# Performance work log

Hardware: AMD Instinct MI355X
Metric: run time of the kernel (lower is better)

## Reference

```python
import jax, jax.numpy as jnp
import numpy as np

B, S, D = 2, 2048, 1024
H = 16
HD = D // H


def setup_inputs() -> dict:
    key = jax.random.key(0)
    k = jax.random.split(key, 5)
    s = 0.02
    return {
        "x": jax.random.normal(k[0], (B, S, D), jnp.float32),
        "w_qkv": jax.random.normal(k[1], (3 * D, D), jnp.float32) * s,
        "b_qkv": jax.random.normal(k[2], (3 * D,), jnp.float32) * s,
        "w_out": jax.random.normal(k[3], (D, D), jnp.float32) * s,
        "b_out": jax.random.normal(k[4], (D,), jnp.float32) * s,
    }


def reference(x, w_qkv, b_qkv, w_out, b_out):
    b, s, d = x.shape
    h, hd = H, HD
    scale = hd ** -0.5
    # QKV projection: [B,S,3D] -> [3,B,H,S,hd]
    qkv = x @ w_qkv.T + b_qkv
    qkv = qkv.reshape(b, s, 3, h, hd).transpose(2, 0, 3, 1, 4)
    q, k, v = qkv[0], qkv[1], qkv[2]
    # Attention scores [B,H,S,S]
    scores = jnp.einsum("bhqd,bhkd->bhqk", q, k) * scale
    attn = jax.nn.softmax(scores, axis=-1)
    # Attend and merge heads
    attended = jnp.einsum("bhqk,bhkd->bqhd", attn, v).reshape(b, s, d)
    return attended @ w_out.T + b_out
```

## Files before the change

kernel.cpp:

```cpp
#include <hip/hip_runtime.h>
#include <hip/hip_bf16.h>

typedef __hip_bfloat16 bf16;
typedef __attribute__((ext_vector_type(8))) short short8;
typedef __attribute__((ext_vector_type(8))) __bf16 bf16x8;
typedef __attribute__((ext_vector_type(4))) float f32x4;
typedef __attribute__((ext_vector_type(16))) float f32x16;
typedef __attribute__((ext_vector_type(4))) unsigned int u32x4;
typedef __attribute__((ext_vector_type(2))) unsigned int u32x2;

#define MFMA16(a, b, c)                                                        \
  __builtin_amdgcn_mfma_f32_16x16x32_bf16(__builtin_bit_cast(bf16x8, (a)),     \
                                          __builtin_bit_cast(bf16x8, (b)),     \
                                          (c), 0, 0, 0)
#define MFMA32(a, b, c)                                                        \
  __builtin_amdgcn_mfma_f32_32x32x16_bf16(__builtin_bit_cast(bf16x8, (a)),     \
                                          __builtin_bit_cast(bf16x8, (b)),     \
                                          (c), 0, 0, 0)

#define GLD16(gsrc, ldst)                                                      \
  __builtin_amdgcn_global_load_lds(                                            \
      (const __attribute__((address_space(1))) void*)(gsrc),                   \
      (__attribute__((address_space(3))) void*)(ldst), 16, 0, 0)

__device__ inline short f2bfs(float f) {
  return __builtin_bit_cast(short, __float2bfloat16(f));
}
__device__ inline unsigned pk2(float lo, float hi) {
  unsigned a = (unsigned short)__builtin_bit_cast(short, __float2bfloat16(lo));
  unsigned b = (unsigned short)__builtin_bit_cast(short, __float2bfloat16(hi));
  return a | (b << 16);
}

template <typename T> __device__ inline short8 ld8bf(const T* p);
template <> __device__ inline short8 ld8bf<bf16>(const bf16* p) {
  return *(const short8*)p;
}
template <> __device__ inline short8 ld8bf<float>(const float* p) {
  f32x4 a = *(const f32x4*)p;
  f32x4 b = *(const f32x4*)(p + 4);
  short8 r;
  r[0] = f2bfs(a[0]); r[1] = f2bfs(a[1]); r[2] = f2bfs(a[2]); r[3] = f2bfs(a[3]);
  r[4] = f2bfs(b[0]); r[5] = f2bfs(b[1]); r[6] = f2bfs(b[2]); r[7] = f2bfs(b[3]);
  return r;
}

template <typename OT> __device__ inline void st1(OT* p, float v);
template <> __device__ inline void st1<bf16>(bf16* p, float v) {
  *p = __float2bfloat16(v);
}
template <> __device__ inline void st1<float>(float* p, float v) { *p = v; }

__device__ inline unsigned int funnel16(unsigned int hi, unsigned int lo) {
  return (unsigned int)(((((unsigned long long)hi) << 32) | lo) >> 16);
}
__device__ inline short8 rotl8(short8 v, int r) {
  u32x4 W = __builtin_bit_cast(u32x4, v);
  u32x4 T, U, F;
  int wr = r >> 1;
  T[0] = (wr & 1) ? W[1] : W[0];
  T[1] = (wr & 1) ? W[2] : W[1];
  T[2] = (wr & 1) ? W[3] : W[2];
  T[3] = (wr & 1) ? W[0] : W[3];
  U[0] = (wr & 2) ? T[2] : T[0];
  U[1] = (wr & 2) ? T[3] : T[1];
  U[2] = (wr & 2) ? T[0] : T[2];
  U[3] = (wr & 2) ? T[1] : T[3];
  F[0] = (r & 1) ? funnel16(U[1], U[0]) : U[0];
  F[1] = (r & 1) ? funnel16(U[2], U[1]) : U[1];
  F[2] = (r & 1) ? funnel16(U[3], U[2]) : U[2];
  F[3] = (r & 1) ? funnel16(U[0], U[3]) : U[3];
  return __builtin_bit_cast(short8, F);
}

__global__ __launch_bounds__(256) void cvt3(
    const float* __restrict__ s0, bf16* __restrict__ d0, int n0,
    const float* __restrict__ s1, bf16* __restrict__ d1, int n1,
    const float* __restrict__ s2, bf16* __restrict__ d2, int n2) {
  int i = (blockIdx.x * 256 + threadIdx.x) * 8;
  if (i < n0) {
    *(short8*)&d0[i] = ld8bf(s0 + i);
  } else if ((i -= n0) < n1) {
    *(short8*)&d1[i] = ld8bf(s1 + i);
  } else if ((i -= n1) < n2) {
    *(short8*)&d2[i] = ld8bf(s2 + i);
  }
}

template <typename OT>
__global__ __launch_bounds__(256, 2) void gemm_lds_bias(
    const bf16* __restrict__ A, const bf16* __restrict__ B,
    const float* __restrict__ bias, OT* __restrict__ C, int M, int N, int K) {
  __shared__ bf16 As[128][64];
  __shared__ bf16 Bs[128][64];

  const int tid = threadIdx.x;
  const int w = tid >> 6, l = tid & 63;
  const int wr = w >> 1, wc = w & 1;
  const int m0 = blockIdx.y * 128, n0 = blockIdx.x * 128;

  f32x4 acc[4][4] = {};

  const int srow = l >> 3;
  const int scol = (l & 7) * 8;

  for (int kt = 0; kt < K; kt += 64) {
#pragma unroll
    for (int j = 0; j < 4; ++j) {
      int chunk = w * 4 + j;
      int row = chunk * 8 + srow;
      GLD16(A + (size_t)(m0 + row) * K + kt + scol, &As[0][0] + chunk * 512);
      GLD16(B + (size_t)(n0 + row) * K + kt + scol, &Bs[0][0] + chunk * 512);
    }
    __syncthreads();

#pragma unroll
    for (int kk = 0; kk < 2; ++kk) {
      short8 af[4], bfv[4];
#pragma unroll
      for (int i = 0; i < 4; ++i) {
        af[i]  = *(const short8*)&As[wr * 64 + i * 16 + (l & 15)]
                                   [kk * 32 + (l >> 4) * 8];
        bfv[i] = *(const short8*)&Bs[wc * 64 + i * 16 + (l & 15)]
                                   [kk * 32 + (l >> 4) * 8];
      }
#pragma unroll
      for (int i = 0; i < 4; ++i)
#pragma unroll
        for (int jn = 0; jn < 4; ++jn)
          acc[i][jn] = MFMA16(af[i], bfv[jn], acc[i][jn]);
    }
    __syncthreads();
  }

#pragma unroll
  for (int i = 0; i < 4; ++i) {
    int rbase = m0 + wr * 64 + i * 16 + (l >> 4) * 4;
#pragma unroll
    for (int jn = 0; jn < 4; ++jn) {
      int col = n0 + wc * 64 + jn * 16 + (l & 15);
      float bv = bias[col];
#pragma unroll
      for (int r = 0; r < 4; ++r)
        st1(&C[(size_t)(rbase + r) * N + col], acc[i][jn][r] + bv);
    }
  }
}

template <typename AT, typename OT>
__global__ __launch_bounds__(256, 2) void gemm_bt_bias(
    const AT* __restrict__ A, const float* __restrict__ B,
    const float* __restrict__ bias, OT* __restrict__ C, int M, int N, int K) {
  __shared__ bf16 As[128][64];
  __shared__ bf16 Bs[128][64];

  const int tid = threadIdx.x;
  const int w = tid >> 6, l = tid & 63;
  const int wr = w >> 1, wc = w & 1;
  const int m0 = blockIdx.y * 128, n0 = blockIdx.x * 128;

  f32x4 acc[4][4] = {};

  const int srow = tid >> 3;
  const int scol = (tid & 7) * 8;

  for (int kt = 0; kt < K; kt += 64) {
    short8 aReg[4], bReg[4];
#pragma unroll
    for (int p = 0; p < 4; ++p) {
      int row = p * 32 + srow;
      aReg[p] = ld8bf(A + (size_t)(m0 + row) * K + kt + scol);
      bReg[p] = ld8bf(B + (size_t)(n0 + row) * K + kt + scol);
    }
    __syncthreads();
#pragma unroll
    for (int p = 0; p < 4; ++p) {
      int row = p * 32 + srow;
      *(short8*)&As[row][scol] = aReg[p];
      *(short8*)&Bs[row][scol] = bReg[p];
    }
    __syncthreads();

#pragma unroll
    for (int kk = 0; kk < 2; ++kk) {
      short8 af[4], bfv[4];
#pragma unroll
      for (int i = 0; i < 4; ++i) {
        af[i]  = *(const short8*)&As[wr * 64 + i * 16 + (l & 15)]
                                   [kk * 32 + (l >> 4) * 8];
        bfv[i] = *(const short8*)&Bs[wc * 64 + i * 16 + (l & 15)]
                                   [kk * 32 + (l >> 4) * 8];
      }
#pragma unroll
      for (int i = 0; i < 4; ++i)
#pragma unroll
        for (int jn = 0; jn < 4; ++jn)
          acc[i][jn] = MFMA16(af[i], bfv[jn], acc[i][jn]);
    }
  }

#pragma unroll
  for (int i = 0; i < 4; ++i) {
    int rbase = m0 + wr * 64 + i * 16 + (l >> 4) * 4;
#pragma unroll
    for (int jn = 0; jn < 4; ++jn) {
      int col = n0 + wc * 64 + jn * 16 + (l & 15);
      float bv = bias[col];
#pragma unroll
      for (int r = 0; r < 4; ++r)
        st1(&C[(size_t)(rbase + r) * N + col], acc[i][jn][r] + bv);
    }
  }
}

__global__ __launch_bounds__(256, 2) void attn_fwd(
    const bf16* __restrict__ qkv, bf16* __restrict__ attended) {
  const int S = 2048, D3 = 3072, D = 1024;
  const int qt = blockIdx.x, bh = blockIdx.y;
  const int b = bh >> 4, h = bh & 15;
  const int tid = threadIdx.x, w = tid >> 6, l = tid & 63;
  const int lo5 = l & 31, hi = l >> 5;

  __shared__ bf16 Klds[64][72];
  __shared__ bf16 Vt[64][72];

  const int q0w = qt * 128 + w * 32;

  short8 qf[4];
  {
    size_t qrow = (size_t)(b * S + q0w + lo5) * D3 + h * 64;
#pragma unroll
    for (int ks = 0; ks < 4; ++ks)
      qf[ks] = *(const short8*)&qkv[qrow + ks * 16 + hi * 8];
  }

  float m_raw = -1e30f, l_i = 0.f;
  f32x16 o0 = {}, o1 = {};

  const float Cs = 0.125f * 1.44269504088896340736f;

  const int srow = tid >> 2;
  const int scq = tid & 3;

  short8 k0, k1, v0, v1;
  {
    size_t gb = (size_t)(b * S + srow) * D3 + h * 64 + scq * 16;
    k0 = *(const short8*)&qkv[gb + 1024];
    k1 = *(const short8*)&qkv[gb + 1024 + 8];
    v0 = *(const short8*)&qkv[gb + 2048];
    v1 = *(const short8*)&qkv[gb + 2048 + 8];
  }

  for (int kv0 = 0; kv0 < S; kv0 += 64) {
    __syncthreads();
    *(short8*)&Klds[srow][scq * 16] = k0;
    *(short8*)&Klds[srow][scq * 16 + 8] = k1;
#pragma unroll
    for (int g = 0; g < 2; ++g) {
      int sI = scq * 2 + g;
      short8 u = rotl8(g ? v1 : v0, sI);
#pragma unroll
      for (int j = 0; j < 8; ++j) {
        int jj = (j + sI) & 7;
        *(short*)&Vt[sI * 8 + jj][srow] = (short)u[j];
      }
    }
    __syncthreads();

    if (kv0 + 64 < S) {
      size_t gb = (size_t)(b * S + kv0 + 64 + srow) * D3 + h * 64 + scq * 16;
      k0 = *(const short8*)&qkv[gb + 1024];
      k1 = *(const short8*)&qkv[gb + 1024 + 8];
      v0 = *(const short8*)&qkv[gb + 2048];
      v1 = *(const short8*)&qkv[gb + 2048 + 8];
    }

    f32x16 s0 = {}, s1 = {};
    __builtin_amdgcn_s_setprio(1);
#pragma unroll
    for (int ks = 0; ks < 4; ++ks) {
      short8 ka0 = *(const short8*)&Klds[lo5][ks * 16 + hi * 8];
      short8 ka1 = *(const short8*)&Klds[32 + lo5][ks * 16 + hi * 8];
      s0 = MFMA32(ka0, qf[ks], s0);
      s1 = MFMA32(ka1, qf[ks], s1);
    }
    __builtin_amdgcn_s_setprio(0);

    f32x16 tm;
#pragma unroll
    for (int r = 0; r < 16; ++r) tm[r] = fmaxf(s0[r], s1[r]);
#pragma unroll
    for (int st = 8; st > 0; st >>= 1)
#pragma unroll
      for (int r = 0; r < st; ++r) tm[r] = fmaxf(tm[r], tm[r + st]);
    float mx = fmaxf(tm[0], __shfl_xor(tm[0], 32));

    bool deferred = __all((mx - m_raw) * Cs <= 8.0f);
    float mn, alpha;
    if (deferred) {
      mn = m_raw;
      alpha = 1.0f;
    } else {
      mn = fmaxf(m_raw, mx);
      alpha = __builtin_amdgcn_exp2f((m_raw - mn) * Cs);
      m_raw = mn;
    }
    float pc = mn * Cs;

    f32x16 e0, e1;
#pragma unroll
    for (int r = 0; r < 16; ++r) {
      e0[r] = __builtin_amdgcn_exp2f(__builtin_fmaf(s0[r], Cs, -pc));
      e1[r] = __builtin_amdgcn_exp2f(__builtin_fmaf(s1[r], Cs, -pc));
    }
    f32x16 ts;
#pragma unroll
    for (int r = 0; r < 16; ++r) ts[r] = e0[r] + e1[r];
#pragma unroll
    for (int st = 8; st > 0; st >>= 1)
#pragma unroll
      for (int r = 0; r < st; ++r) ts[r] += ts[r + st];
    float sf = ts[0] + __shfl_xor(ts[0], 32);
    if (deferred) {
      l_i += sf;
    } else {
      l_i = l_i * alpha + sf;
      o0 *= alpha;
      o1 *= alpha;
    }

    unsigned po[2][4][2];
#pragma unroll
    for (int t = 0; t < 4; ++t) {
      po[0][t][0] = pk2(e0[4 * t], e0[4 * t + 1]);
      po[0][t][1] = pk2(e0[4 * t + 2], e0[4 * t + 3]);
      po[1][t][0] = pk2(e1[4 * t], e1[4 * t + 1]);
      po[1][t][1] = pk2(e1[4 * t + 2], e1[4 * t + 3]);
    }
    unsigned pr[2][2][2];
#pragma unroll
    for (int g = 0; g < 2; ++g)
#pragma unroll
      for (int p = 0; p < 2; ++p)
#pragma unroll
        for (int hf = 0; hf < 2; ++hf) {
          unsigned y = hi ? po[g][2 * p][hf] : po[g][2 * p + 1][hf];
          pr[g][p][hf] = (unsigned)__shfl_xor((int)y, 32);
        }

    __builtin_amdgcn_s_setprio(1);
#pragma unroll
    for (int ks = 0; ks < 4; ++ks) {
      const int g = ks >> 1, p = ks & 1;
      u32x4 fw;
      fw[0] = hi ? pr[g][p][0] : po[g][2 * p][0];
      fw[1] = hi ? pr[g][p][1] : po[g][2 * p][1];
      fw[2] = hi ? po[g][2 * p + 1][0] : pr[g][p][0];
      fw[3] = hi ? po[g][2 * p + 1][1] : pr[g][p][1];
      short8 pf = __builtin_bit_cast(short8, fw);
      short8 va0 = *(const short8*)&Vt[lo5][ks * 16 + hi * 8];
      short8 va1 = *(const short8*)&Vt[32 + lo5][ks * 16 + hi * 8];
      o0 = MFMA32(va0, pf, o0);
      o1 = MFMA32(va1, pf, o1);
    }
    __builtin_amdgcn_s_setprio(0);
  }

  float inv = 1.0f / l_i;
  size_t orow = (size_t)(b * S + q0w + lo5) * D + h * 64;
#pragma unroll
  for (int t = 0; t < 4; ++t) {
    u32x2 w0, w1;
    w0[0] = pk2(o0[4 * t] * inv, o0[4 * t + 1] * inv);
    w0[1] = pk2(o0[4 * t + 2] * inv, o0[4 * t + 3] * inv);
    w1[0] = pk2(o1[4 * t] * inv, o1[4 * t + 1] * inv);
    w1[1] = pk2(o1[4 * t + 2] * inv, o1[4 * t + 3] * inv);
    *(u32x2*)&attended[orow + 8 * t + 4 * hi] = w0;
    *(u32x2*)&attended[orow + 32 + 8 * t + 4 * hi] = w1;
  }
}

extern "C" void kernel_launch(void* const* d_in, const int* in_sizes, int n_in,
                              void* d_out, int out_size, void* d_ws,
                              size_t ws_size, hipStream_t stream) {
  const float* x     = (const float*)d_in[0];
  const float* w_qkv = (const float*)d_in[1];
  const float* b_qkv = (const float*)d_in[2];
  const float* w_out = (const float*)d_in[3];
  const float* b_out = (const float*)d_in[4];
  float* out = (float*)d_out;

  const int BS = 4096;
  const int D = 1024, D3 = 3072;
  const int NX = BS * D, NWQ = D3 * D, NWO = D * D;

  bf16* qkv = (bf16*)d_ws;
  bf16* att = qkv + (size_t)BS * D3;

  const size_t NEED = ((size_t)BS * D3 + (size_t)BS * D + (size_t)D3 * D +
                       (size_t)D * D) * sizeof(bf16);

  if (ws_size >= NEED) {
    bf16* xb  = att;
    bf16* wqb = xb + (size_t)NX;
    bf16* wob = wqb + (size_t)NWQ;

    int ncvt = (NX + NWQ + NWO) / 8;
    cvt3<<<(ncvt + 255) / 256, 256, 0, stream>>>(x, xb, NX, w_qkv, wqb, NWQ,
                                                 w_out, wob, NWO);
    gemm_lds_bias<bf16><<<dim3(D3 / 128, BS / 128), 256, 0, stream>>>(
        xb, wqb, b_qkv, qkv, BS, D3, D);
    attn_fwd<<<dim3(16, 32), 256, 0, stream>>>(qkv, att);
    gemm_lds_bias<float><<<dim3(D / 128, BS / 128), 256, 0, stream>>>(
        att, wob, b_out, out, BS, D, D);
  } else {
    gemm_bt_bias<float, bf16><<<dim3(D3 / 128, BS / 128), 256, 0, stream>>>(
        x, w_qkv, b_qkv, qkv, BS, D3, D);
    attn_fwd<<<dim3(16, 32), 256, 0, stream>>>(qkv, att);
    gemm_bt_bias<bf16, float><<<dim3(D / 128, BS / 128), 256, 0, stream>>>(
        att, w_out, b_out, out, BS, D, D);
  }
}
```

Baseline: 130.5 us.

## Double-buffer K/V tiles in LDS and remap attention block order

Switches the attention kernel from a single K/V LDS tile with two barriers per iteration to a double-buffered ping-pong. Each iteration writes the next tile into the alternate buffer and prefetches the tile after that into registers, needing only one barrier. It also remaps the flat block index so blocks are spread across heads and batches, likely for better cache or XCD locality. This doubles LDS use to about 36KB per block, which may affect occupancy at 2 blocks per CU.

Result: slower. 142.6 us (+9.3%).

```diff
diff --git a/kernel.cpp b/kernel.cpp
--- a/kernel.cpp
+++ b/kernel.cpp
@@ -216,13 +216,15 @@
 __global__ __launch_bounds__(256, 2) void attn_fwd(
     const bf16* __restrict__ qkv, bf16* __restrict__ attended) {
   const int S = 2048, D3 = 3072, D = 1024;
-  const int qt = blockIdx.x, bh = blockIdx.y;
+  const int flat = blockIdx.y * 16 + blockIdx.x;
+  const int n = (flat & 7) * 64 + (flat >> 3);
+  const int qt = n & 15, bh = n >> 4;
   const int b = bh >> 4, h = bh & 15;
   const int tid = threadIdx.x, w = tid >> 6, l = tid & 63;
   const int lo5 = l & 31, hi = l >> 5;
 
-  __shared__ bf16 Klds[64][72];
-  __shared__ bf16 Vt[64][72];
+  __shared__ bf16 K2[2][64][72];
+  __shared__ bf16 V2[2][64][72];
 
   const int q0w = qt * 128 + w * 32;
 
@@ -241,46 +243,68 @@
 
   const int srow = tid >> 2;
   const int scq = tid & 3;
+  const size_t gstep = (size_t)(b * S + srow) * D3 + h * 64 + scq * 16;
 
   short8 k0, k1, v0, v1;
   {
-    size_t gb = (size_t)(b * S + srow) * D3 + h * 64 + scq * 16;
-    k0 = *(const short8*)&qkv[gb + 1024];
-    k1 = *(const short8*)&qkv[gb + 1024 + 8];
-    v0 = *(const short8*)&qkv[gb + 2048];
-    v1 = *(const short8*)&qkv[gb + 2048 + 8];
-  }
-
-  for (int kv0 = 0; kv0 < S; kv0 += 64) {
+    const bf16* g = qkv + gstep;
+    k0 = *(const short8*)&g[1024];
+    k1 = *(const short8*)&g[1024 + 8];
+    v0 = *(const short8*)&g[2048];
+    v1 = *(const short8*)&g[2048 + 8];
+  }
+  *(short8*)&K2[0][srow][scq * 16] = k0;
+  *(short8*)&K2[0][srow][scq * 16 + 8] = k1;
+#pragma unroll
+  for (int g = 0; g < 2; ++g) {
+    int sI = scq * 2 + g;
+    short8 u = rotl8(g ? v1 : v0, sI);
+#pragma unroll
+    for (int j = 0; j < 8; ++j) {
+      int jj = (j + sI) & 7;
+      *(short*)&V2[0][sI * 8 + jj][srow] = (short)u[j];
+    }
+  }
+  {
+    const bf16* g = qkv + gstep + (size_t)64 * D3;
+    k0 = *(const short8*)&g[1024];
+    k1 = *(const short8*)&g[1024 + 8];
+    v0 = *(const short8*)&g[2048];
+    v1 = *(const short8*)&g[2048 + 8];
+  }
+
+  for (int t = 0; t < 32; ++t) {
+    const int cur = t & 1;
     __syncthreads();
-    *(short8*)&Klds[srow][scq * 16] = k0;
-    *(short8*)&Klds[srow][scq * 16 + 8] = k1;
-#pragma unroll
-    for (int g = 0; g < 2; ++g) {
-      int sI = scq * 2 + g;
-      short8 u = rotl8(g ? v1 : v0, sI);
-#pragma unroll
-      for (int j = 0; j < 8; ++j) {
-        int jj = (j + sI) & 7;
-        *(short*)&Vt[sI * 8 + jj][srow] = (short)u[j];
+
+    if (t + 1 < 32) {
+      *(short8*)&K2[cur ^ 1][srow][scq * 16] = k0;
+      *(short8*)&K2[cur ^ 1][srow][scq * 16 + 8] = k1;
+#pragma unroll
+      for (int g = 0; g < 2; ++g) {
+        int sI = scq * 2 + g;
+        short8 u = rotl8(g ? v1 : v0, sI);
+#pragma unroll
+        for (int j = 0; j < 8; ++j) {
+          int jj = (j + sI) & 7;
+          *(short*)&V2[cur ^ 1][sI * 8 + jj][srow] = (short)u[j];
+        }
       }
-    }
-    __syncthreads();
-
-    if (kv0 + 64 < S) {
-      size_t gb = (size_t)(b * S + kv0 + 64 + srow) * D3 + h * 64 + scq * 16;
-      k0 = *(const short8*)&qkv[gb + 1024];
-      k1 = *(const short8*)&qkv[gb + 1024 + 8];
-      v0 = *(const short8*)&qkv[gb + 2048];
-      v1 = *(const short8*)&qkv[gb + 2048 + 8];
+      if (t + 2 < 32) {
+        const bf16* g = qkv + gstep + (size_t)(t + 2) * 64 * D3;
+        k0 = *(const short8*)&g[1024];
+        k1 = *(const short8*)&g[1024 + 8];
+        v0 = *(const short8*)&g[2048];
+        v1 = *(const short8*)&g[2048 + 8];
+      }
     }
 
     f32x16 s0 = {}, s1 = {};
     __builtin_amdgcn_s_setprio(1);
 #pragma unroll
     for (int ks = 0; ks < 4; ++ks) {
-      short8 ka0 = *(const short8*)&Klds[lo5][ks * 16 + hi * 8];
-      short8 ka1 = *(const short8*)&Klds[32 + lo5][ks * 16 + hi * 8];
+      short8 ka0 = *(const short8*)&K2[cur][lo5][ks * 16 + hi * 8];
+      short8 ka1 = *(const short8*)&K2[cur][32 + lo5][ks * 16 + hi * 8];
       s0 = MFMA32(ka0, qf[ks], s0);
       s1 = MFMA32(ka1, qf[ks], s1);
     }
@@ -331,11 +355,11 @@
 
     unsigned po[2][4][2];
 #pragma unroll
-    for (int t = 0; t < 4; ++t) {
-      po[0][t][0] = pk2(e0[4 * t], e0[4 * t + 1]);
-      po[0][t][1] = pk2(e0[4 * t + 2], e0[4 * t + 3]);
-      po[1][t][0] = pk2(e1[4 * t], e1[4 * t + 1]);
-      po[1][t][1] = pk2(e1[4 * t + 2], e1[4 * t + 3]);
+    for (int tq = 0; tq < 4; ++tq) {
+      po[0][tq][0] = pk2(e0[4 * tq], e0[4 * tq + 1]);
+      po[0][tq][1] = pk2(e0[4 * tq + 2], e0[4 * tq + 3]);
+      po[1][tq][0] = pk2(e1[4 * tq], e1[4 * tq + 1]);
+      po[1][tq][1] = pk2(e1[4 * tq + 2], e1[4 * tq + 3]);
     }
     unsigned pr[2][2][2];
 #pragma unroll
@@ -358,8 +382,8 @@
       fw[2] = hi ? po[g][2 * p + 1][0] : pr[g][p][0];
       fw[3] = hi ? po[g][2 * p + 1][1] : pr[g][p][1];
       short8 pf = __builtin_bit_cast(short8, fw);
-      short8 va0 = *(const short8*)&Vt[lo5][ks * 16 + hi * 8];
-      short8 va1 = *(const short8*)&Vt[32 + lo5][ks * 16 + hi * 8];
+      short8 va0 = *(const short8*)&V2[cur][lo5][ks * 16 + hi * 8];
+      short8 va1 = *(const short8*)&V2[cur][32 + lo5][ks * 16 + hi * 8];
       o0 = MFMA32(va0, pf, o0);
       o1 = MFMA32(va1, pf, o1);
     }
```

## Double KV tile to 128 keys per iteration and remap block order

Applied to the files above, without the earlier changes.

The attention kernel now processes 128 keys per loop iteration instead of 64, which halves the number of barriers and online-softmax rescale steps. The V prefetch is split out and issued after the QK MFMAs, so loads are staggered across the iteration. Block indices are also remapped so neighbouring workgroups are spread across heads and batches, which changes L2 locality for K/V. In exchange, LDS and register use per block grow, which may reduce occupancy under launch_bounds(256,2).

After: 127.3 us. 2.5% less time.

```diff
diff --git a/kernel.cpp b/kernel.cpp
--- a/kernel.cpp
+++ b/kernel.cpp
@@ -216,13 +216,15 @@
 __global__ __launch_bounds__(256, 2) void attn_fwd(
     const bf16* __restrict__ qkv, bf16* __restrict__ attended) {
   const int S = 2048, D3 = 3072, D = 1024;
-  const int qt = blockIdx.x, bh = blockIdx.y;
+  const int flat = blockIdx.y * 16 + blockIdx.x;
+  const int n = (flat & 7) * 64 + (flat >> 3);
+  const int qt = n & 15, bh = n >> 4;
   const int b = bh >> 4, h = bh & 15;
   const int tid = threadIdx.x, w = tid >> 6, l = tid & 63;
   const int lo5 = l & 31, hi = l >> 5;
 
-  __shared__ bf16 Klds[64][72];
-  __shared__ bf16 Vt[64][72];
+  __shared__ bf16 Klds[128][72];
+  __shared__ bf16 Vt[64][136];
 
   const int q0w = qt * 128 + w * 32;
 
@@ -241,54 +243,86 @@
 
   const int srow = tid >> 2;
   const int scq = tid & 3;
-
-  short8 k0, k1, v0, v1;
+  const size_t gb0 = (size_t)(b * S + srow) * D3 + h * 64 + scq * 16;
+  const size_t HSTEP = (size_t)64 * D3;
+
+  short8 k0, k1, k2, k3, v0, v1, v2, v3;
   {
-    size_t gb = (size_t)(b * S + srow) * D3 + h * 64 + scq * 16;
-    k0 = *(const short8*)&qkv[gb + 1024];
-    k1 = *(const short8*)&qkv[gb + 1024 + 8];
-    v0 = *(const short8*)&qkv[gb + 2048];
-    v1 = *(const short8*)&qkv[gb + 2048 + 8];
-  }
-
-  for (int kv0 = 0; kv0 < S; kv0 += 64) {
+    const bf16* g = qkv + gb0;
+    k0 = *(const short8*)&g[1024];
+    k1 = *(const short8*)&g[1024 + 8];
+    v0 = *(const short8*)&g[2048];
+    v1 = *(const short8*)&g[2048 + 8];
+    const bf16* g2 = g + HSTEP;
+    k2 = *(const short8*)&g2[1024];
+    k3 = *(const short8*)&g2[1024 + 8];
+    v2 = *(const short8*)&g2[2048];
+    v3 = *(const short8*)&g2[2048 + 8];
+  }
+
+#define PACKP(G, SV)                                                           \
+  {                                                                            \
+    _Pragma("unroll") for (int tq = 0; tq < 4; ++tq) {                         \
+      po[G][tq][0] = pk2((SV)[4 * tq], (SV)[4 * tq + 1]);                      \
+      po[G][tq][1] = pk2((SV)[4 * tq + 2], (SV)[4 * tq + 3]);                  \
+    }                                                                          \
+  }
+
+  for (int t = 0; t < 16; ++t) {
     __syncthreads();
     *(short8*)&Klds[srow][scq * 16] = k0;
     *(short8*)&Klds[srow][scq * 16 + 8] = k1;
+    *(short8*)&Klds[64 + srow][scq * 16] = k2;
+    *(short8*)&Klds[64 + srow][scq * 16 + 8] = k3;
 #pragma unroll
     for (int g = 0; g < 2; ++g) {
       int sI = scq * 2 + g;
-      short8 u = rotl8(g ? v1 : v0, sI);
+      short8 ua = rotl8(g ? v1 : v0, sI);
+      short8 ub = rotl8(g ? v3 : v2, sI);
 #pragma unroll
       for (int j = 0; j < 8; ++j) {
         int jj = (j + sI) & 7;
-        *(short*)&Vt[sI * 8 + jj][srow] = (short)u[j];
+        *(short*)&Vt[sI * 8 + jj][srow] = (short)ua[j];
+        *(short*)&Vt[sI * 8 + jj][64 + srow] = (short)ub[j];
       }
     }
     __syncthreads();
 
-    if (kv0 + 64 < S) {
-      size_t gb = (size_t)(b * S + kv0 + 64 + srow) * D3 + h * 64 + scq * 16;
-      k0 = *(const short8*)&qkv[gb + 1024];
-      k1 = *(const short8*)&qkv[gb + 1024 + 8];
-      v0 = *(const short8*)&qkv[gb + 2048];
-      v1 = *(const short8*)&qkv[gb + 2048 + 8];
-    }
-
-    f32x16 s0 = {}, s1 = {};
+    if (t + 1 < 16) {
+      const bf16* g = qkv + gb0 + (size_t)(t + 1) * 2 * HSTEP;
+      k0 = *(const short8*)&g[1024];
+      k1 = *(const short8*)&g[1024 + 8];
+      k2 = *(const short8*)&g[HSTEP + 1024];
+      k3 = *(const short8*)&g[HSTEP + 1024 + 8];
+    }
+
+    f32x16 s0 = {}, s1 = {}, s2 = {}, s3 = {};
     __builtin_amdgcn_s_setprio(1);
 #pragma unroll
     for (int ks = 0; ks < 4; ++ks) {
-      short8 ka0 = *(const short8*)&Klds[lo5][ks * 16 + hi * 8];
-      short8 ka1 = *(const short8*)&Klds[32 + lo5][ks * 16 + hi * 8];
-      s0 = MFMA32(ka0, qf[ks], s0);
-      s1 = MFMA32(ka1, qf[ks], s1);
+      short8 km0 = *(const short8*)&Klds[lo5][ks * 16 + hi * 8];
+      short8 km1 = *(const short8*)&Klds[32 + lo5][ks * 16 + hi * 8];
+      short8 km2 = *(const short8*)&Klds[64 + lo5][ks * 16 + hi * 8];
+      short8 km3 = *(const short8*)&Klds[96 + lo5][ks * 16 + hi * 8];
+      s0 = MFMA32(km0, qf[ks], s0);
+      s1 = MFMA32(km1, qf[ks], s1);
+      s2 = MFMA32(km2, qf[ks], s2);
+      s3 = MFMA32(km3, qf[ks], s3);
     }
     __builtin_amdgcn_s_setprio(0);
 
+    if (t + 1 < 16) {
+      const bf16* g = qkv + gb0 + (size_t)(t + 1) * 2 * HSTEP;
+      v0 = *(const short8*)&g[2048];
+      v1 = *(const short8*)&g[2048 + 8];
+      v2 = *(const short8*)&g[HSTEP + 2048];
+      v3 = *(const short8*)&g[HSTEP + 2048 + 8];
+    }
+
     f32x16 tm;
 #pragma unroll
-    for (int r = 0; r < 16; ++r) tm[r] = fmaxf(s0[r], s1[r]);
+    for (int r = 0; r < 16; ++r)
+      tm[r] = fmaxf(fmaxf(s0[r], s1[r]), fmaxf(s2[r], s3[r]));
 #pragma unroll
     for (int st = 8; st > 0; st >>= 1)
 #pragma unroll
@@ -307,15 +341,17 @@
     }
     float pc = mn * Cs;
 
-    f32x16 e0, e1;
 #pragma unroll
     for (int r = 0; r < 16; ++r) {
-      e0[r] = __builtin_amdgcn_exp2f(__builtin_fmaf(s0[r], Cs, -pc));
-      e1[r] = __builtin_amdgcn_exp2f(__builtin_fmaf(s1[r], Cs, -pc));
+      s0[r] = __builtin_amdgcn_exp2f(__builtin_fmaf(s0[r], Cs, -pc));
+      s1[r] = __builtin_amdgcn_exp2f(__builtin_fmaf(s1[r], Cs, -pc));
+      s2[r] = __builtin_amdgcn_exp2f(__builtin_fmaf(s2[r], Cs, -pc));
+      s3[r] = __builtin_amdgcn_exp2f(__builtin_fmaf(s3[r], Cs, -pc));
     }
     f32x16 ts;
 #pragma unroll
-    for (int r = 0; r < 16; ++r) ts[r] = e0[r] + e1[r];
+    for (int r = 0; r < 16; ++r)
+      ts[r] = (s0[r] + s1[r]) + (s2[r] + s3[r]);
 #pragma unroll
     for (int st = 8; st > 0; st >>= 1)
 #pragma unroll
@@ -329,17 +365,11 @@
       o1 *= alpha;
     }
 
-    unsigned po[2][4][2];
-#pragma unroll
-    for (int t = 0; t < 4; ++t) {
-      po[0][t][0] = pk2(e0[4 * t], e0[4 * t + 1]);
-      po[0][t][1] = pk2(e0[4 * t + 2], e0[4 * t + 3]);
-      po[1][t][0] = pk2(e1[4 * t], e1[4 * t + 1]);
-      po[1][t][1] = pk2(e1[4 * t + 2], e1[4 * t + 3]);
-    }
-    unsigned pr[2][2][2];
-#pragma unroll
-    for (int g = 0; g < 2; ++g)
+    unsigned po[4][4][2];
+    PACKP(0, s0) PACKP(1, s1) PACKP(2, s2) PACKP(3, s3)
+    unsigned pr[4][2][2];
+#pragma unroll
+    for (int g = 0; g < 4; ++g)
 #pragma unroll
       for (int p = 0; p < 2; ++p)
 #pragma unroll
@@ -350,16 +380,16 @@
 
     __builtin_amdgcn_s_setprio(1);
 #pragma unroll
-    for (int ks = 0; ks < 4; ++ks) {
-      const int g = ks >> 1, p = ks & 1;
+    for (int ks2 = 0; ks2 < 8; ++ks2) {
+      const int g = ks2 >> 1, p = ks2 & 1;
       u32x4 fw;
       fw[0] = hi ? pr[g][p][0] : po[g][2 * p][0];
       fw[1] = hi ? pr[g][p][1] : po[g][2 * p][1];
       fw[2] = hi ? po[g][2 * p + 1][0] : pr[g][p][0];
       fw[3] = hi ? po[g][2 * p + 1][1] : pr[g][p][1];
       short8 pf = __builtin_bit_cast(short8, fw);
-      short8 va0 = *(const short8*)&Vt[lo5][ks * 16 + hi * 8];
-      short8 va1 = *(const short8*)&Vt[32 + lo5][ks * 16 + hi * 8];
+      short8 va0 = *(const short8*)&Vt[lo5][ks2 * 16 + hi * 8];
+      short8 va1 = *(const short8*)&Vt[32 + lo5][ks2 * 16 + hi * 8];
       o0 = MFMA32(va0, pf, o0);
       o1 = MFMA32(va1, pf, o1);
     }
```
